# Optimization experiments

Measured on AMD Instinct MI355X. Metric: run time of the kernel, lower is better.

The kernel has to match this reference:

```python
import jax, jax.numpy as jnp
import numpy as np

HEADS = 8

def _grid_edges(H, W):
    # 4-neighbor grid adjacency, built at trace time (static), faithful to the torch double loop
    N = H * W
    idx = np.arange(N).reshape(H, W)
    e = np.zeros((N, N), np.float32)
    a, b = idx[1:, :].ravel(), idx[:-1, :].ravel()
    e[a, b] = 1.0; e[b, a] = 1.0
    a, b = idx[:, 1:].ravel(), idx[:, :-1].ravel()
    e[a, b] = 1.0; e[b, a] = 1.0
    return jnp.asarray(e)

def _layernorm(x, g, b, eps=1e-5):
    m = x.mean(-1, keepdims=True)
    v = x.var(-1, keepdims=True)
    return (x - m) / jnp.sqrt(v + eps) * g + b

def _gat(nodes, edges, W, b, rel):
    # nodes: [N,B,E]; W: [4,E,E] (q,k,v,out); rel: [HEADS]
    N, B, E = nodes.shape
    hd = E // HEADS
    q = (nodes @ W[0].T + b[0]).reshape(N, B, HEADS, hd)
    k = (nodes @ W[1].T + b[1]).reshape(N, B, HEADS, hd)
    v = (nodes @ W[2].T + b[2]).reshape(N, B, HEADS, hd)
    s = jnp.einsum('ibhd,jbhd->hbij', q, k) / float(np.sqrt(hd))
    s = s + edges[None, None] * rel[:, None, None, None]  # per-head edge relation bias
    a = jax.nn.softmax(s, axis=1)  # faithful to source: softmax over dim=1 (batch axis)
    o = jnp.einsum('hbij,jbhd->ibhd', a, v).reshape(N, B, E)
    return o @ W[3].T + b[3]

def _mha(q_in, kv_in, W, b):
    # standard nn.MultiheadAttention (eval, no dropout); seq-first [L,B,E]
    L, B, E = q_in.shape
    S = kv_in.shape[0]
    hd = E // HEADS
    q = (q_in @ W[0].T + b[0]).reshape(L, B, HEADS, hd)
    k = (kv_in @ W[1].T + b[1]).reshape(S, B, HEADS, hd)
    v = (kv_in @ W[2].T + b[2]).reshape(S, B, HEADS, hd)
    s = jnp.einsum('ibhd,jbhd->hbij', q, k) / float(np.sqrt(hd))
    a = jax.nn.softmax(s, axis=-1)
    o = jnp.einsum('hbij,jbhd->ibhd', a, v).reshape(L, B, E)
    return o @ W[3].T + b[3]

def reference(x, gat_W, gat_b, gat_rel, cross_W, cross_b, ln_g, ln_b):
    B, C, H, W = x.shape
    P = H // 4
    # global nodes: avg_pool2d(kernel=4) then flatten to [P*P, B, C]
    g = x.reshape(B, C, P, 4, P, 4).mean(axis=(3, 5))
    global_nodes = g.reshape(B, C, P * P).transpose(2, 0, 1)
    global_edges = jnp.ones((P * P, P * P), x.dtype)
    local_nodes = x.reshape(B, C, H * W).transpose(2, 0, 1)  # [HW,B,C]
    local_edges = _grid_edges(H, W)
    g_out = _gat(global_nodes, global_edges, gat_W[0], gat_b[0], gat_rel[0])
    g_out = _layernorm(g_out + global_nodes, ln_g[0], ln_b[0])
    l_out = _gat(local_nodes, local_edges, gat_W[1], gat_b[1], gat_rel[1])
    l_out = _layernorm(l_out + local_nodes, ln_g[1], ln_b[1])
    # nearest upsample x4 of global output back to HxW
    g_map = g_out.transpose(1, 2, 0).reshape(B, C, P, P)
    g_up = jnp.repeat(jnp.repeat(g_map, 4, axis=2), 4, axis=3)
    g_up = g_up.reshape(B, C, H * W).transpose(2, 0, 1)
    c_out = _mha(l_out, g_up, cross_W, cross_b)
    c_out = _layernorm(c_out + l_out, ln_g[2], ln_b[2])
    return c_out.transpose(1, 2, 0).reshape(B, C, H, W)

def setup_inputs() -> dict:
    key = jax.random.key(0)
    ks = jax.random.split(key, 6)
    B, C, H, W = 2, 256, 40, 40
    E = C
    sc = 0.02
    return {
        "x": jax.random.normal(ks[0], (B, C, H, W), jnp.float32),
        "gat_W": jax.random.normal(ks[1], (2, 4, E, E), jnp.float32) * sc,
        "gat_b": jax.random.normal(ks[2], (2, 4, E), jnp.float32) * sc,
        "gat_rel": jax.random.normal(ks[3], (2, HEADS), jnp.float32),
        "cross_W": jax.random.normal(ks[4], (4, E, E), jnp.float32) * sc,
        "cross_b": jax.random.normal(ks[5], (4, E), jnp.float32) * sc,
        "ln_g": jnp.ones((3, E), jnp.float32),
        "ln_b": jnp.zeros((3, E), jnp.float32),
    }
```

## Files before the change

### kernel.cpp

```cpp
#include <hip/hip_runtime.h>
#include <math.h>

#define NLOC 1600
#define NGLO 100

typedef unsigned short u16;
typedef short s16x8 __attribute__((ext_vector_type(8)));
typedef float f32x4 __attribute__((ext_vector_type(4)));

__device__ __forceinline__ short f2bf(float f) {
    unsigned u = __float_as_uint(f);
    u += 0x7fffu + ((u >> 16) & 1u);
    return (short)(u >> 16);
}
__device__ __forceinline__ float bf2f(u16 h) {
    return __uint_as_float(((unsigned)h) << 16);
}

__global__ __launch_bounds__(256) void wconv_kernel(const float* __restrict__ w1,
                                                    const float* __restrict__ w2,
                                                    u16* __restrict__ d1,
                                                    u16* __restrict__ d2) {
    int t = blockIdx.x * 256 + threadIdx.x;
    const float* src; u16* dst; int idx;
    if (t < 131072) { src = w1; dst = d1; idx = t; }
    else            { src = w2; dst = d2; idx = t - 131072; }
    float4 v = ((const float4*)src)[idx];
    ushort4 o;
    o.x = (u16)f2bf(v.x); o.y = (u16)f2bf(v.y);
    o.z = (u16)f2bf(v.z); o.w = (u16)f2bf(v.w);
    ((ushort4*)dst)[idx] = o;
}

__global__ __launch_bounds__(256) void prep_kernel(const float* __restrict__ x,
                                                   float* __restrict__ nodes,
                                                   u16* __restrict__ nodesb,
                                                   float* __restrict__ gn,
                                                   u16* __restrict__ gnb) {
    int bid = blockIdx.x;
    if (bid < 3200) {
        int t = bid * 256 + threadIdx.x;
        int c = t & 255;
        int b = (t >> 8) & 1;
        int n = t >> 9;
        float v = x[((size_t)(b * 256 + c)) * 1600 + n];
        nodes[t] = v;
        nodesb[t] = (u16)f2bf(v);
    } else {
        int t = (bid - 3200) * 256 + threadIdx.x;
        int c = t & 255;
        int b = (t >> 8) & 1;
        int n = t >> 9;
        int p = n / 10, qq = n - p * 10;
        const float* xp = x + ((size_t)(b * 256 + c)) * 1600 + (p * 4) * 40 + qq * 4;
        float s = 0.f;
#pragma unroll
        for (int dy = 0; dy < 4; ++dy)
#pragma unroll
            for (int dx = 0; dx < 4; ++dx)
                s += xp[dy * 40 + dx];
        s *= (1.f / 16.f);
        gn[t] = s;
        gnb[t] = (u16)f2bf(s);
    }
}

template <bool BF16OUT>
__global__ __launch_bounds__(64) void gemm_mfma(const u16* __restrict__ A,
                                                const u16* __restrict__ W,
                                                const float* __restrict__ bias,
                                                void* __restrict__ Cout, int M) {
    int z = blockIdx.z;
    W    += (size_t)z * 65536;
    bias += (size_t)z * 256;
    int lane = threadIdx.x;
    int c = lane & 15, qd = lane >> 4;
    int m0 = blockIdx.x * 32, n0 = blockIdx.y * 64;
    size_t co = (size_t)z * M * 256;

    f32x4 acc[2][4] = {};
#pragma unroll 2
    for (int kc = 0; kc < 8; ++kc) {
        int ko = kc * 32 + qd * 8;
        s16x8 af[2], bf[4];
#pragma unroll
        for (int mi = 0; mi < 2; ++mi) {
            int row = m0 + mi * 16 + c;
            s16x8 zz = {};
            af[mi] = (row < M) ? *(const s16x8*)(A + (size_t)row * 256 + ko) : zz;
        }
#pragma unroll
        for (int ni = 0; ni < 4; ++ni)
            bf[ni] = *(const s16x8*)(W + (size_t)(n0 + ni * 16 + c) * 256 + ko);
#pragma unroll
        for (int mi = 0; mi < 2; ++mi)
#pragma unroll
            for (int ni = 0; ni < 4; ++ni)
                acc[mi][ni] = __builtin_amdgcn_mfma_f32_16x16x32_bf16(af[mi], bf[ni],
                                                                      acc[mi][ni], 0, 0, 0);
    }
#pragma unroll
    for (int mi = 0; mi < 2; ++mi) {
#pragma unroll
        for (int r = 0; r < 4; ++r) {
            int row = m0 + mi * 16 + 4 * qd + r;
            if (row < M) {
#pragma unroll
                for (int ni = 0; ni < 4; ++ni) {
                    int col = n0 + ni * 16 + c;
                    float val = acc[mi][ni][r] + bias[col];
                    if (BF16OUT)
                        ((u16*)Cout)[co + (size_t)row * 256 + col] = (u16)f2bf(val);
                    else
                        ((float*)Cout)[co + (size_t)row * 256 + col] = val;
                }
            }
        }
    }
}

__global__ __launch_bounds__(256) void vtrans_kernel(const u16* __restrict__ src,
                                                     u16* __restrict__ dst,
                                                     int M, int Npad) {
    __shared__ u16 tile[32][33];
    int m0 = blockIdx.x * 32;
    int e0 = blockIdx.y * 32;
    int tx = threadIdx.x & 31, ty = threadIdx.x >> 5;
#pragma unroll
    for (int k2 = 0; k2 < 4; ++k2) {
        int m = m0 + ty + k2 * 8;
        tile[ty + k2 * 8][tx] = (m < M) ? src[(size_t)m * 256 + e0 + tx] : (u16)0;
    }
    __syncthreads();
    int b = tx >> 4, nl = tx & 15;
    int n = (m0 >> 1) + nl;
    if (n < Npad) {
#pragma unroll
        for (int k2 = 0; k2 < 4; ++k2) {
            int e = e0 + ty + k2 * 8;
            dst[(size_t)(b * 256 + e) * Npad + n] = tile[2 * nl + b][ty + k2 * 8];
        }
    }
}

__global__ __launch_bounds__(64) void colsum_kernel(const u16* __restrict__ vt,
                                                    float* __restrict__ sumv1,
                                                    int Npad) {
    int e = blockIdx.x;
    const u16* row = vt + (size_t)(256 + e) * Npad;
    float s = 0.f;
    for (int n = threadIdx.x; n < Npad; n += 64) s += bf2f(row[n]);
#pragma unroll
    for (int off = 1; off < 64; off <<= 1) s += __shfl_xor(s, off);
    if (threadIdx.x == 0) sumv1[e] = s;
}

struct KV { s16x8 kf[2][2]; s16x8 vf[2][2]; };

__global__ __launch_bounds__(64) void gat_attn_mfma(
    const u16* __restrict__ qb, const u16* __restrict__ kb,
    const u16* __restrict__ vt, const float* __restrict__ sumv1,
    u16* __restrict__ out, int N, int Npad, int nIT)
{
    __shared__ short At[16][40];
    int lane = threadIdx.x;
    int c  = lane & 15;
    int qd = lane >> 4;
    int h  = blockIdx.x / nIT;
    int it = blockIdx.x - h * nIT;
    int i0 = it * 16;
    int hb = h * 32;

    s16x8 qf0 = {}, qf1 = {};
    int i = i0 + c;
    if (i < N) {
        const u16* qp = qb + ((size_t)i * 2) * 256 + hb + qd * 8;
        qf0 = *(const s16x8*)qp;
        qf1 = *(const s16x8*)(qp + 256);
    }
#pragma unroll
    for (int z = 0; z < 8; ++z) qf0[z] ^= (short)0x8000;

    f32x4 o0[2] = {};
    f32x4 t1[2] = {};

    auto load_kv = [&](KV& B, int j0) {
#pragma unroll
        for (int b = 0; b < 2; ++b)
#pragma unroll
            for (int js = 0; js < 2; ++js) {
                int j = j0 + js * 16 + c;
                s16x8 kv = {};
                if (j < N) kv = *(const s16x8*)(kb + ((size_t)j * 2 + b) * 256 + hb + qd * 8);
                B.kf[b][js] = kv;
            }
#pragma unroll
        for (int b = 0; b < 2; ++b)
#pragma unroll
            for (int dh = 0; dh < 2; ++dh)
                B.vf[b][dh] = *(const s16x8*)(vt + (size_t)(b * 256 + hb + dh * 16 + c) * Npad
                                              + j0 + qd * 8);
    };

    auto compute = [&](KV& B) {
        f32x4 z4 = {};
        f32x4 sd0 = __builtin_amdgcn_mfma_f32_16x16x32_bf16(qf0, B.kf[0][0], z4, 0, 0, 0);
        sd0       = __builtin_amdgcn_mfma_f32_16x16x32_bf16(qf1, B.kf[1][0], sd0, 0, 0, 0);
        f32x4 sd1 = __builtin_amdgcn_mfma_f32_16x16x32_bf16(qf0, B.kf[0][1], z4, 0, 0, 0);
        sd1       = __builtin_amdgcn_mfma_f32_16x16x32_bf16(qf1, B.kf[1][1], sd1, 0, 0, 0);
#pragma unroll
        for (int r = 0; r < 4; ++r) {
            float e0v = __expf(sd0[r] * 0.17677669529663687f);
            At[4 * qd + r][c]      = f2bf(__builtin_amdgcn_rcpf(1.f + e0v));
            float e1v = __expf(sd1[r] * 0.17677669529663687f);
            At[4 * qd + r][16 + c] = f2bf(__builtin_amdgcn_rcpf(1.f + e1v));
        }
        asm volatile("s_waitcnt lgkmcnt(0)" ::: "memory");
        s16x8 af = *(const s16x8*)&At[c][qd * 8];
        o0[0] = __builtin_amdgcn_mfma_f32_16x16x32_bf16(af, B.vf[0][0], o0[0], 0, 0, 0);
        o0[1] = __builtin_amdgcn_mfma_f32_16x16x32_bf16(af, B.vf[0][1], o0[1], 0, 0, 0);
        t1[0] = __builtin_amdgcn_mfma_f32_16x16x32_bf16(af, B.vf[1][0], t1[0], 0, 0, 0);
        t1[1] = __builtin_amdgcn_mfma_f32_16x16x32_bf16(af, B.vf[1][1], t1[1], 0, 0, 0);
    };

    KV B0, B1;
    load_kv(B0, 0);
    for (int j0 = 0; j0 < N; j0 += 64) {
        bool h1 = (j0 + 32 < N);
        if (h1) load_kv(B1, j0 + 32);
        compute(B0);
        if (h1) {
            if (j0 + 64 < N) load_kv(B0, j0 + 64);
            compute(B1);
        }
    }

#pragma unroll
    for (int dh = 0; dh < 2; ++dh) {
        float sv = sumv1[hb + dh * 16 + c];
#pragma unroll
        for (int r = 0; r < 4; ++r) {
            int ii = i0 + 4 * qd + r;
            if (ii < N) {
                size_t o = ((size_t)ii * 2) * 256 + hb + dh * 16 + c;
                out[o]       = (u16)f2bf(o0[dh][r]);
                out[o + 256] = (u16)f2bf(sv - t1[dh][r]);
            }
        }
    }
}

__global__ __launch_bounds__(256) void lgat_attn(
    const u16* __restrict__ qb, const u16* __restrict__ kb,
    const u16* __restrict__ vt, float* __restrict__ pO, float* __restrict__ pT)
{
    __shared__ u16 ks[2][32][40];
    __shared__ u16 vs[2][32][40];
    __shared__ short At[4][16][40];

    int tid = threadIdx.x;
    int w = tid >> 6, lane = tid & 63;
    int c = lane & 15, qd = lane >> 4;
    int bx = blockIdx.x;
    int q4 = bx & 3;
    int hic = bx >> 2;
    int ic = hic % 25, h = hic / 25;
    int hb = h * 32;
    int i0 = ic * 64 + w * 16;
    int jb0 = q4 * 13, jbe = (jb0 + 13 < 50) ? jb0 + 13 : 50;

    const u16* qp = qb + ((size_t)(i0 + c) * 2) * 256 + hb + qd * 8;
    s16x8 qf0 = *(const s16x8*)qp;
    s16x8 qf1 = *(const s16x8*)(qp + 256);
#pragma unroll
    for (int z = 0; z < 8; ++z) qf0[z] ^= (short)0x8000;

    f32x4 o0[2] = {}, t1[2] = {};

    int srow = tid >> 2, part = tid & 3;
    int sjl = srow >> 1, sb = srow & 1;
    int vb_ = srow >> 5, vd = srow & 31;

    for (int jb = jb0; jb < jbe; ++jb) {
        int j0 = jb * 32;
        __syncthreads();
        {
            s16x8 kv = *(const s16x8*)(kb + (size_t)(j0 + sjl) * 512 + sb * 256 + hb + part * 8);
            *(s16x8*)&ks[sb][sjl][part * 8] = kv;
            s16x8 vv = *(const s16x8*)(vt + (size_t)(vb_ * 256 + hb + vd) * 1600 + j0 + part * 8);
            *(s16x8*)&vs[vb_][vd][part * 8] = vv;
        }
        __syncthreads();

        s16x8 kf00 = *(const s16x8*)&ks[0][c][qd * 8];
        s16x8 kf10 = *(const s16x8*)&ks[1][c][qd * 8];
        s16x8 kf01 = *(const s16x8*)&ks[0][16 + c][qd * 8];
        s16x8 kf11 = *(const s16x8*)&ks[1][16 + c][qd * 8];

        f32x4 z4 = {};
        f32x4 sd0 = __builtin_amdgcn_mfma_f32_16x16x32_bf16(qf0, kf00, z4, 0, 0, 0);
        sd0       = __builtin_amdgcn_mfma_f32_16x16x32_bf16(qf1, kf10, sd0, 0, 0, 0);
        f32x4 sd1 = __builtin_amdgcn_mfma_f32_16x16x32_bf16(qf0, kf01, z4, 0, 0, 0);
        sd1       = __builtin_amdgcn_mfma_f32_16x16x32_bf16(qf1, kf11, sd1, 0, 0, 0);
#pragma unroll
        for (int r = 0; r < 4; ++r) {
            float e0v = __expf(sd0[r] * 0.17677669529663687f);
            At[w][4 * qd + r][c]      = f2bf(__builtin_amdgcn_rcpf(1.f + e0v));
            float e1v = __expf(sd1[r] * 0.17677669529663687f);
            At[w][4 * qd + r][16 + c] = f2bf(__builtin_amdgcn_rcpf(1.f + e1v));
        }
        asm volatile("s_waitcnt lgkmcnt(0)" ::: "memory");
        s16x8 af = *(const s16x8*)&At[w][c][qd * 8];

        s16x8 vf00 = *(const s16x8*)&vs[0][c][qd * 8];
        s16x8 vf01 = *(const s16x8*)&vs[0][16 + c][qd * 8];
        s16x8 vf10 = *(const s16x8*)&vs[1][c][qd * 8];
        s16x8 vf11 = *(const s16x8*)&vs[1][16 + c][qd * 8];

        o0[0] = __builtin_amdgcn_mfma_f32_16x16x32_bf16(af, vf00, o0[0], 0, 0, 0);
        o0[1] = __builtin_amdgcn_mfma_f32_16x16x32_bf16(af, vf01, o0[1], 0, 0, 0);
        t1[0] = __builtin_amdgcn_mfma_f32_16x16x32_bf16(af, vf10, t1[0], 0, 0, 0);
        t1[1] = __builtin_amdgcn_mfma_f32_16x16x32_bf16(af, vf11, t1[1], 0, 0, 0);
    }

    size_t base = (size_t)q4 * 409600;
#pragma unroll
    for (int dh = 0; dh < 2; ++dh)
#pragma unroll
        for (int r = 0; r < 4; ++r) {
            size_t idx = base + (size_t)(i0 + 4 * qd + r) * 256 + hb + dh * 16 + c;
            pO[idx] = o0[dh][r];
            pT[idx] = t1[dh][r];
        }
}

__global__ __launch_bounds__(256) void lgat_combine(const float* __restrict__ pO,
                                                    const float* __restrict__ pT,
                                                    const float* __restrict__ sumv1,
                                                    u16* __restrict__ out) {
    int t = blockIdx.x * 256 + threadIdx.x;
    int e = t & 255;
    int i = t >> 8;
    float o  = pO[t] + pO[t + 409600] + pO[t + 819200] + pO[t + 1228800];
    float tt = pT[t] + pT[t + 409600] + pT[t + 819200] + pT[t + 1228800];
    out[(size_t)i * 512 + e]       = (u16)f2bf(o);
    out[(size_t)i * 512 + 256 + e] = (u16)f2bf(sumv1[e] - tt);
}

__global__ __launch_bounds__(64) void cross_attn_mfma(
    const u16* __restrict__ qb, const u16* __restrict__ kb,
    const u16* __restrict__ vt, u16* __restrict__ out)
{
    __shared__ short At[16][136];
    int lane = threadIdx.x;
    int c  = lane & 15;
    int qd = lane >> 4;
    int bx = blockIdx.x;
    int it = bx % 100;
    int hb2 = bx / 100;
    int h = hb2 >> 1, b = hb2 & 1;
    int i0 = it * 16;
    int hb = h * 32;

    for (int z = lane; z < 16 * 24; z += 64)
        At[z / 24][112 + (z % 24)] = 0;

    const u16* qp = qb + ((size_t)(i0 + c) * 2 + b) * 256 + hb + qd * 8;
    s16x8 qf = *(const s16x8*)qp;

    f32x4 s[7];
#pragma unroll
    for (int jt = 0; jt < 7; ++jt) {
        int j = jt * 16 + c;
        s16x8 kf = {};
        if (j < NGLO) kf = *(const s16x8*)(kb + ((size_t)j * 2 + b) * 256 + hb + qd * 8);
        f32x4 z4 = {};
        s[jt] = __builtin_amdgcn_mfma_f32_16x16x32_bf16(qf, kf, z4, 0, 0, 0);
    }
    if (c >= 4) {
#pragma unroll
// ... 19 lines not shown
        for (int jt = 0; jt < 7; ++jt) {
            float p = __expf(s[jt][r] - mm);
            s[jt][r] = p;
            ll += p;
        }
        ll += __shfl_xor(ll, 1);
        ll += __shfl_xor(ll, 2);
        ll += __shfl_xor(ll, 4);
        ll += __shfl_xor(ll, 8);
        l[r] = ll;
    }
#pragma unroll
    for (int jt = 0; jt < 7; ++jt)
#pragma unroll
        for (int r = 0; r < 4; ++r)
            At[4 * qd + r][jt * 16 + c] = f2bf(s[jt][r]);
    asm volatile("s_waitcnt lgkmcnt(0)" ::: "memory");

    f32x4 o[2] = {};
#pragma unroll
    for (int kc = 0; kc < 4; ++kc) {
        s16x8 af = *(const s16x8*)&At[c][kc * 32 + qd * 8];
#pragma unroll
        for (int dh = 0; dh < 2; ++dh) {
            s16x8 vf = *(const s16x8*)(vt + (size_t)(b * 256 + hb + dh * 16 + c) * 128
                                       + kc * 32 + qd * 8);
            o[dh] = __builtin_amdgcn_mfma_f32_16x16x32_bf16(af, vf, o[dh], 0, 0, 0);
        }
    }
#pragma unroll
    for (int dh = 0; dh < 2; ++dh)
#pragma unroll
        for (int r = 0; r < 4; ++r) {
            int ii = i0 + 4 * qd + r;
            out[((size_t)ii * 2 + b) * 256 + hb + dh * 16 + c] = (u16)f2bf(o[dh][r] / l[r]);
        }
}

__global__ __launch_bounds__(256) void ln_kernel(const float* __restrict__ P,
                                                 const float* __restrict__ R,
                                                 const float* __restrict__ g,
                                                 const float* __restrict__ bb,
                                                 float* __restrict__ out,
                                                 u16* __restrict__ outb, int mode) {
    int r = blockIdx.x;
    int c = threadIdx.x;
    size_t o = (size_t)r * 256 + c;
    float x = P[o] + R[o];
    float s1 = x, s2 = x * x;
#pragma unroll
    for (int off = 1; off < 64; off <<= 1) {
        s1 += __shfl_xor(s1, off);
        s2 += __shfl_xor(s2, off);
    }
    __shared__ float w1[4], w2[4];
    int wid = c >> 6;
    if ((c & 63) == 0) { w1[wid] = s1; w2[wid] = s2; }
    __syncthreads();
    s1 = w1[0] + w1[1] + w1[2] + w1[3];
    s2 = w2[0] + w2[1] + w2[2] + w2[3];
    float mean = s1 * (1.f / 256.f);
    float var  = s2 * (1.f / 256.f) - mean * mean;
    float y = (x - mean) * rsqrtf(var + 1e-5f) * g[c] + bb[c];
    if (mode == 0) {
        out[o] = y;
        if (outb) outb[o] = (u16)f2bf(y);
    } else {
        int n = r >> 1, b = r & 1;
        out[((size_t)(b * 256 + c)) * 1600 + n] = y;
    }
}

extern "C" void kernel_launch(void* const* d_in, const int* in_sizes, int n_in,
                              void* d_out, int out_size, void* d_ws, size_t ws_size,
                              hipStream_t stream) {
    const float* x        = (const float*)d_in[0];
    const float* gat_W    = (const float*)d_in[1];
    const float* gat_b    = (const float*)d_in[2];
    const float* cross_W  = (const float*)d_in[4];
    const float* cross_b  = (const float*)d_in[5];
    const float* ln_g     = (const float*)d_in[6];
    const float* ln_b     = (const float*)d_in[7];
    float* out = (float*)d_out;

    float* ws    = (float*)d_ws;
// ... 22 lines not shown
    u16* gvt    = gvb + 51200;
    u16* gattb  = gvt + 65536;
    u16* goutb  = gattb + 51200;
    u16* ckb    = goutb + 51200;
    u16* cvb    = ckb + 51200;
    u16* cvt    = cvb + 51200;
    u16* loutb  = vbuf;
    u16* cqb    = attb;
    u16* cattb  = kbuf;

    const u16* W0b = wgatb;
    const u16* W1b = wgatb + 4 * 65536;
    const float* b0 = gat_b;
    const float* b1 = gat_b + 4 * 256;

    wconv_kernel<<<768, 256, 0, stream>>>(gat_W, cross_W, wgatb, wcrsb);
    prep_kernel<<<3400, 256, 0, stream>>>(x, nodes, nodesb, gn, gnb);

    gemm_mfma<true><<<dim3(7, 4, 3), 64, 0, stream>>>(gnb, W0b, b0, gqb, 200);
    vtrans_kernel<<<dim3(8, 8), 256, 0, stream>>>(gvb, gvt, 200, 128);
    colsum_kernel<<<256, 64, 0, stream>>>(gvt, sv1g, 128);
    gat_attn_mfma<<<8 * 7, 64, 0, stream>>>(gqb, gkb, gvt, sv1g, gattb, NGLO, 128, 7);
    gemm_mfma<false><<<dim3(7, 4, 1), 64, 0, stream>>>(gattb, W0b + 3 * 65536, b0 + 768, gprj, 200);
    ln_kernel<<<200, 256, 0, stream>>>(gprj, gn, ln_g, ln_b, gout, goutb, 0);

    gemm_mfma<true><<<dim3(100, 4, 3), 64, 0, stream>>>(nodesb, W1b, b1, qbuf, 3200);
    vtrans_kernel<<<dim3(100, 8), 256, 0, stream>>>(vbuf, vtb, 3200, 1600);
    colsum_kernel<<<256, 64, 0, stream>>>(vtb, sv1l, 1600);
    lgat_attn<<<800, 256, 0, stream>>>(qbuf, kbuf, vtb, pO, pT);
    lgat_combine<<<1600, 256, 0, stream>>>(pO, pT, sv1l, attb);
    gemm_mfma<false><<<dim3(100, 4, 1), 64, 0, stream>>>(attb, W1b + 3 * 65536, b1 + 768, proj, 3200);
    ln_kernel<<<3200, 256, 0, stream>>>(proj, nodes, ln_g + 256, ln_b + 256, lout, loutb, 0);

    gemm_mfma<true><<<dim3(100, 4, 1), 64, 0, stream>>>(loutb, wcrsb, cross_b, cqb, 3200);
    gemm_mfma<true><<<dim3(7, 4, 2), 64, 0, stream>>>(goutb, wcrsb + 1 * 65536, cross_b + 256, ckb, 200);
    vtrans_kernel<<<dim3(8, 8), 256, 0, stream>>>(cvb, cvt, 200, 128);
    cross_attn_mfma<<<1600, 64, 0, stream>>>(cqb, ckb, cvt, cattb);
    gemm_mfma<false><<<dim3(100, 4, 1), 64, 0, stream>>>(cattb, wcrsb + 3 * 65536, cross_b + 768, proj, 3200);
    ln_kernel<<<3200, 256, 0, stream>>>(proj, lout, ln_g + 512, ln_b + 512, out, (u16*)0, 1);
}
```

Baseline: 201.5 us.

## Fuse pipeline into fewer kernels with GEMM+LayerNorm epilogues and merged branches

Collapses about twenty launches into nine by merging the global and local branches into shared grids. The column sums move into the V-transpose via atomics, and the output projections are fused with residual add and LayerNorm in a full-row per-wave GEMM epilogue. The cross attention now packs four waves per block. This cuts launch overhead and the fp32 intermediate round trips through memory. In exchange, the projection+LN kernels run on very few blocks (for example 50 or 64), which may underuse the GPU.

```diff
diff --git a/kernel.cpp b/kernel.cpp
--- a/kernel.cpp
+++ b/kernel.cpp
@@ -17,27 +17,135 @@
     return __uint_as_float(((unsigned)h) << 16);
 }
 
-__global__ __launch_bounds__(256) void wconv_kernel(const float* __restrict__ w1,
-                                                    const float* __restrict__ w2,
-                                                    u16* __restrict__ d1,
-                                                    u16* __restrict__ d2) {
-    int t = blockIdx.x * 256 + threadIdx.x;
-    const float* src; u16* dst; int idx;
-    if (t < 131072) { src = w1; dst = d1; idx = t; }
-    else            { src = w2; dst = d2; idx = t - 131072; }
-    float4 v = ((const float4*)src)[idx];
-    ushort4 o;
-    o.x = (u16)f2bf(v.x); o.y = (u16)f2bf(v.y);
-    o.z = (u16)f2bf(v.z); o.w = (u16)f2bf(v.w);
-    ((ushort4*)dst)[idx] = o;
-}
-
-__global__ __launch_bounds__(256) void prep_kernel(const float* __restrict__ x,
-                                                   float* __restrict__ nodes,
-                                                   u16* __restrict__ nodesb,
-                                                   float* __restrict__ gn,
-                                                   u16* __restrict__ gnb) {
-    int bid = blockIdx.x;
+
+__device__ __forceinline__ void gemm_tile(int lane, const u16* __restrict__ A,
+                                          const u16* __restrict__ W,
+                                          const float* __restrict__ bias,
+                                          u16* __restrict__ C, int M, int m0, int n0) {
+    int c = lane & 15, qd = lane >> 4;
+    f32x4 acc[2][4] = {};
+#pragma unroll 2
+    for (int kc = 0; kc < 8; ++kc) {
+        int ko = kc * 32 + qd * 8;
+        s16x8 af[2], bf[4];
+#pragma unroll
+        for (int mi = 0; mi < 2; ++mi) {
+            int row = m0 + mi * 16 + c;
+            s16x8 zz = {};
+            af[mi] = (row < M) ? *(const s16x8*)(A + (size_t)row * 256 + ko) : zz;
+        }
+#pragma unroll
+        for (int ni = 0; ni < 4; ++ni)
+            bf[ni] = *(const s16x8*)(W + (size_t)(n0 + ni * 16 + c) * 256 + ko);
+#pragma unroll
+        for (int mi = 0; mi < 2; ++mi)
+#pragma unroll
+            for (int ni = 0; ni < 4; ++ni)
+                acc[mi][ni] = __builtin_amdgcn_mfma_f32_16x16x32_bf16(af[mi], bf[ni],
+                                                                      acc[mi][ni], 0, 0, 0);
+    }
+#pragma unroll
+    for (int mi = 0; mi < 2; ++mi)
+#pragma unroll
+        for (int r = 0; r < 4; ++r) {
+            int row = m0 + mi * 16 + 4 * qd + r;
+            if (row < M) {
+#pragma unroll
+                for (int ni = 0; ni < 4; ++ni) {
+                    int col = n0 + ni * 16 + c;
+                    C[(size_t)row * 256 + col] = (u16)f2bf(acc[mi][ni][r] + bias[col]);
+                }
+            }
+        }
+}
+
+__device__ __forceinline__ void gemmln_wave(int lane, const u16* __restrict__ A,
+                                            const u16* __restrict__ W,
+                                            const float* __restrict__ bias,
+                                            const float* __restrict__ R,
+                                            const float* __restrict__ g,
+                                            const float* __restrict__ bb,
+                                            float* fout, u16* bfout, float* dout,
+                                            int M, int m0, int mode) {
+    int c = lane & 15, qd = lane >> 4;
+    f32x4 acc[16] = {};
+#pragma unroll 2
+    for (int kc = 0; kc < 8; ++kc) {
+        int ko = kc * 32 + qd * 8;
+        int row = m0 + c;
+        s16x8 zz = {};
+        s16x8 af = (row < M) ? *(const s16x8*)(A + (size_t)row * 256 + ko) : zz;
+#pragma unroll
+        for (int ni = 0; ni < 16; ++ni) {
+            s16x8 bf = *(const s16x8*)(W + (size_t)(ni * 16 + c) * 256 + ko);
+            acc[ni] = __builtin_amdgcn_mfma_f32_16x16x32_bf16(af, bf, acc[ni], 0, 0, 0);
+        }
+    }
+#pragma unroll
+    for (int r = 0; r < 4; ++r) {
+        int row = m0 + 4 * qd + r;
+        bool ok = (row < M);
+        float v[16];
+        float s1 = 0.f, s2 = 0.f;
+#pragma unroll
+        for (int ni = 0; ni < 16; ++ni) {
+            int col = ni * 16 + c;
+            float val = acc[ni][r] + bias[col] + (ok ? R[(size_t)row * 256 + col] : 0.f);
+            v[ni] = val;
+            s1 += val; s2 += val * val;
+        }
+        s1 += __shfl_xor(s1, 1); s2 += __shfl_xor(s2, 1);
+        s1 += __shfl_xor(s1, 2); s2 += __shfl_xor(s2, 2);
+        s1 += __shfl_xor(s1, 4); s2 += __shfl_xor(s2, 4);
+        s1 += __shfl_xor(s1, 8); s2 += __shfl_xor(s2, 8);
+        float mean = s1 * (1.f / 256.f);
+        float var  = s2 * (1.f / 256.f) - mean * mean;
+        float rstd = rsqrtf(var + 1e-5f);
+        if (ok) {
+            if (mode == 0) {
+#pragma unroll
+                for (int ni = 0; ni < 16; ++ni) {
+                    int col = ni * 16 + c;
+                    float y = (v[ni] - mean) * rstd * g[col] + bb[col];
+                    fout[(size_t)row * 256 + col] = y;
+                    bfout[(size_t)row * 256 + col] = (u16)f2bf(y);
+                }
+            } else {
+                int n = row >> 1, b = row & 1;
+#pragma unroll
+                for (int ni = 0; ni < 16; ++ni) {
+                    int col = ni * 16 + c;
+                    float y = (v[ni] - mean) * rstd * g[col] + bb[col];
+                    dout[((size_t)(b * 256 + col)) * 1600 + n] = y;
+                }
+            }
+        }
+    }
+}
+
+__global__ __launch_bounds__(256) void k_prep(const float* __restrict__ gw,
+                                              const float* __restrict__ cw,
+                                              u16* __restrict__ gwb,
+                                              u16* __restrict__ cwb,
+                                              const float* __restrict__ x,
+                                              float* __restrict__ nodes,
+                                              u16* __restrict__ nodesb,
+                                              float* __restrict__ gn,
+                                              u16* __restrict__ gnb) {
+    int bx = blockIdx.x;
+    if (bx < 768) {
+        int t = bx * 256 + threadIdx.x;
+        const float* src; u16* dst; int idx;
+        if (t < 131072) { src = gw; dst = gwb; idx = t; }
+        else            { src = cw; dst = cwb; idx = t - 131072; }
+        float4 v = ((const float4*)src)[idx];
+        ushort4 o;
+        o.x = (u16)f2bf(v.x); o.y = (u16)f2bf(v.y);
+        o.z = (u16)f2bf(v.z); o.w = (u16)f2bf(v.w);
+        ((ushort4*)dst)[idx] = o;
+        return;
+    }
+    int bid = bx - 768;
     if (bid < 3200) {
         int t = bid * 256 + threadIdx.x;
         int c = t & 255;
@@ -65,66 +173,37 @@
     }
 }
 
-template <bool BF16OUT>
-__global__ __launch_bounds__(64) void gemm_mfma(const u16* __restrict__ A,
-                                                const u16* __restrict__ W,
-                                                const float* __restrict__ bias,
-                                                void* __restrict__ Cout, int M) {
-    int z = blockIdx.z;
-    W    += (size_t)z * 65536;
-    bias += (size_t)z * 256;
+__global__ __launch_bounds__(64) void k_qkv(const u16* __restrict__ nodesb,
+                                            const u16* __restrict__ gnb,
+                                            const u16* __restrict__ W1b,
+                                            const u16* __restrict__ W0b,
+                                            const float* __restrict__ b1,
+                                            const float* __restrict__ b0,
+                                            u16* __restrict__ qbuf,
+                                            u16* __restrict__ gqb,
+                                            float* __restrict__ sv1) {
     int lane = threadIdx.x;
-    int c = lane & 15, qd = lane >> 4;
-    int m0 = blockIdx.x * 32, n0 = blockIdx.y * 64;
-    size_t co = (size_t)z * M * 256;
-
-    f32x4 acc[2][4] = {};
-#pragma unroll 2
-    for (int kc = 0; kc < 8; ++kc) {
-        int ko = kc * 32 + qd * 8;
-        s16x8 af[2], bf[4];
-#pragma unroll
-        for (int mi = 0; mi < 2; ++mi) {
-            int row = m0 + mi * 16 + c;
-            s16x8 zz = {};
-            af[mi] = (row < M) ? *(const s16x8*)(A + (size_t)row * 256 + ko) : zz;
-        }
-#pragma unroll
-        for (int ni = 0; ni < 4; ++ni)
-            bf[ni] = *(const s16x8*)(W + (size_t)(n0 + ni * 16 + c) * 256 + ko);
-#pragma unroll
-        for (int mi = 0; mi < 2; ++mi)
-#pragma unroll
-            for (int ni = 0; ni < 4; ++ni)
-                acc[mi][ni] = __builtin_amdgcn_mfma_f32_16x16x32_bf16(af[mi], bf[ni],
-                                                                      acc[mi][ni], 0, 0, 0);
-    }
-#pragma unroll
-    for (int mi = 0; mi < 2; ++mi) {
-#pragma unroll
-        for (int r = 0; r < 4; ++r) {
-            int row = m0 + mi * 16 + 4 * qd + r;
-            if (row < M) {
-#pragma unroll
-                for (int ni = 0; ni < 4; ++ni) {
-                    int col = n0 + ni * 16 + c;
-                    float val = acc[mi][ni][r] + bias[col];
-                    if (BF16OUT)
-                        ((u16*)Cout)[co + (size_t)row * 256 + col] = (u16)f2bf(val);
-                    else
-                        ((float*)Cout)[co + (size_t)row * 256 + col] = val;
-                }
-            }
-        }
-    }
-}
-
-__global__ __launch_bounds__(256) void vtrans_kernel(const u16* __restrict__ src,
-                                                     u16* __restrict__ dst,
-                                                     int M, int Npad) {
+    int bx = blockIdx.x, z = blockIdx.z;
+    int n0 = blockIdx.y * 64;
+    if (bx == 100 && blockIdx.y == 0 && z == 0) {
+#pragma unroll
+        for (int i = 0; i < 8; ++i) sv1[lane * 8 + i] = 0.f;
+    }
+    if (bx < 100)
+        gemm_tile(lane, nodesb, W1b + (size_t)z * 65536, b1 + z * 256,
+                  qbuf + (size_t)z * 819200, 3200, bx * 32, n0);
+    else
+        gemm_tile(lane, gnb, W0b + (size_t)z * 65536, b0 + z * 256,
+                  gqb + (size_t)z * 51200, 200, (bx - 100) * 32, n0);
+}
+
+__device__ __forceinline__ void vtrans_block(const u16* __restrict__ src,
+                                             u16* __restrict__ dst,
+                                             int M, int Npad, int bxx, int byy,
+                                             float* sum) {
     __shared__ u16 tile[32][33];
-    int m0 = blockIdx.x * 32;
-    int e0 = blockIdx.y * 32;
+    int m0 = bxx * 32;
+    int e0 = byy * 32;
     int tx = threadIdx.x & 31, ty = threadIdx.x >> 5;
 #pragma unroll
     for (int k2 = 0; k2 < 4; ++k2) {
@@ -141,229 +220,296 @@
             dst[(size_t)(b * 256 + e) * Npad + n] = tile[2 * nl + b][ty + k2 * 8];
         }
     }
-}
-
-__global__ __launch_bounds__(64) void colsum_kernel(const u16* __restrict__ vt,
-                                                    float* __restrict__ sumv1,
-                                                    int Npad) {
-    int e = blockIdx.x;
-    const u16* row = vt + (size_t)(256 + e) * Npad;
-    float s = 0.f;
-    for (int n = threadIdx.x; n < Npad; n += 64) s += bf2f(row[n]);
-#pragma unroll
-    for (int off = 1; off < 64; off <<= 1) s += __shfl_xor(s, off);
-    if (threadIdx.x == 0) sumv1[e] = s;
-}
-
-struct KV { s16x8 kf[2][2]; s16x8 vf[2][2]; };
-
-__global__ __launch_bounds__(64) void gat_attn_mfma(
+    if (threadIdx.x < 32) {
+        float s = 0.f;
+#pragma unroll
+        for (int r = 0; r < 16; ++r) s += bf2f(tile[2 * r + 1][threadIdx.x]);
+        atomicAdd(&sum[e0 + threadIdx.x], s);
+    }
+}
+
+__global__ __launch_bounds__(256) void k_vtrans(const u16* __restrict__ vbuf,
+                                                u16* __restrict__ vtb,
+                                                const u16* __restrict__ gvb,
+                                                u16* __restrict__ gvt,
+                                                float* __restrict__ sv1l,
+                                                float* __restrict__ sv1g) {
+    int bx = blockIdx.x;
+    if (bx < 100) vtrans_block(vbuf, vtb, 3200, 1600, bx, blockIdx.y, sv1l);
+    else          vtrans_block(gvb, gvt, 200, 128, bx - 100, blockIdx.y, sv1g);
+}
+
+__global__ __launch_bounds__(256) void k_attn(
     const u16* __restrict__ qb, const u16* __restrict__ kb,
-    const u16* __restrict__ vt, const float* __restrict__ sumv1,
-    u16* __restrict__ out, int N, int Npad, int nIT)
-{
-    __shared__ short At[16][40];
-    int lane = threadIdx.x;
-    int c  = lane & 15;
-    int qd = lane >> 4;
-    int h  = blockIdx.x / nIT;
-    int it = blockIdx.x - h * nIT;
-    int i0 = it * 16;
-    int hb = h * 32;
-
-    s16x8 qf0 = {}, qf1 = {};
-    int i = i0 + c;
-    if (i < N) {
-        const u16* qp = qb + ((size_t)i * 2) * 256 + hb + qd * 8;
-        qf0 = *(const s16x8*)qp;
-        qf1 = *(const s16x8*)(qp + 256);
-    }
-#pragma unroll
-    for (int z = 0; z < 8; ++z) qf0[z] ^= (short)0x8000;
-
-    f32x4 o0[2] = {};
-    f32x4 t1[2] = {};
-
-    auto load_kv = [&](KV& B, int j0) {
-#pragma unroll
-        for (int b = 0; b < 2; ++b)
-#pragma unroll
-            for (int js = 0; js < 2; ++js) {
-                int j = j0 + js * 16 + c;
-                s16x8 kv = {};
-                if (j < N) kv = *(const s16x8*)(kb + ((size_t)j * 2 + b) * 256 + hb + qd * 8);
-                B.kf[b][js] = kv;
-            }
-#pragma unroll
-        for (int b = 0; b < 2; ++b)
-#pragma unroll
-            for (int dh = 0; dh < 2; ++dh)
-                B.vf[b][dh] = *(const s16x8*)(vt + (size_t)(b * 256 + hb + dh * 16 + c) * Npad
-                                              + j0 + qd * 8);
-    };
-
-    auto compute = [&](KV& B) {
-        f32x4 z4 = {};
-        f32x4 sd0 = __builtin_amdgcn_mfma_f32_16x16x32_bf16(qf0, B.kf[0][0], z4, 0, 0, 0);
-        sd0       = __builtin_amdgcn_mfma_f32_16x16x32_bf16(qf1, B.kf[1][0], sd0, 0, 0, 0);
-        f32x4 sd1 = __builtin_amdgcn_mfma_f32_16x16x32_bf16(qf0, B.kf[0][1], z4, 0, 0, 0);
-        sd1       = __builtin_amdgcn_mfma_f32_16x16x32_bf16(qf1, B.kf[1][1], sd1, 0, 0, 0);
-#pragma unroll
-        for (int r = 0; r < 4; ++r) {
-            float e0v = __expf(sd0[r] * 0.17677669529663687f);
-            At[4 * qd + r][c]      = f2bf(__builtin_amdgcn_rcpf(1.f + e0v));
-            float e1v = __expf(sd1[r] * 0.17677669529663687f);
-            At[4 * qd + r][16 + c] = f2bf(__builtin_amdgcn_rcpf(1.f + e1v));
-        }
-        asm volatile("s_waitcnt lgkmcnt(0)" ::: "memory");
-        s16x8 af = *(const s16x8*)&At[c][qd * 8];
-        o0[0] = __builtin_amdgcn_mfma_f32_16x16x32_bf16(af, B.vf[0][0], o0[0], 0, 0, 0);
-        o0[1] = __builtin_amdgcn_mfma_f32_16x16x32_bf16(af, B.vf[0][1], o0[1], 0, 0, 0);
-        t1[0] = __builtin_amdgcn_mfma_f32_16x16x32_bf16(af, B.vf[1][0], t1[0], 0, 0, 0);
-        t1[1] = __builtin_amdgcn_mfma_f32_16x16x32_bf16(af, B.vf[1][1], t1[1], 0, 0, 0);
-    };
-
-    KV B0, B1;
-    load_kv(B0, 0);
-    for (int j0 = 0; j0 < N; j0 += 64) {
-        bool h1 = (j0 + 32 < N);
-        if (h1) load_kv(B1, j0 + 32);
-        compute(B0);
-        if (h1) {
-            if (j0 + 64 < N) load_kv(B0, j0 + 64);
-            compute(B1);
-        }
-    }
-
-#pragma unroll
-    for (int dh = 0; dh < 2; ++dh) {
-        float sv = sumv1[hb + dh * 16 + c];
-#pragma unroll
-        for (int r = 0; r < 4; ++r) {
-            int ii = i0 + 4 * qd + r;
-            if (ii < N) {
-                size_t o = ((size_t)ii * 2) * 256 + hb + dh * 16 + c;
-                out[o]       = (u16)f2bf(o0[dh][r]);
-                out[o + 256] = (u16)f2bf(sv - t1[dh][r]);
-            }
-        }
-    }
-}
-
-__global__ __launch_bounds__(256) void lgat_attn(
-    const u16* __restrict__ qb, const u16* __restrict__ kb,
-    const u16* __restrict__ vt, float* __restrict__ pO, float* __restrict__ pT)
+    const u16* __restrict__ vt, float* __restrict__ pO, float* __restrict__ pT,
+    const u16* __restrict__ gqb, const u16* __restrict__ gkb,
+    const u16* __restrict__ gvt, const float* __restrict__ sv1g,
+    u16* __restrict__ gattb)
 {
     __shared__ u16 ks[2][32][40];
     __shared__ u16 vs[2][32][40];
-    __shared__ short At[4][16][40];
+    __shared__ short At4[4][16][40];
 
     int tid = threadIdx.x;
     int w = tid >> 6, lane = tid & 63;
     int c = lane & 15, qd = lane >> 4;
     int bx = blockIdx.x;
-    int q4 = bx & 3;
-    int hic = bx >> 2;
-    int ic = hic % 25, h = hic / 25;
-    int hb = h * 32;
-    int i0 = ic * 64 + w * 16;
-    int jb0 = q4 * 13, jbe = (jb0 + 13 < 50) ? jb0 + 13 : 50;
-
-    const u16* qp = qb + ((size_t)(i0 + c) * 2) * 256 + hb + qd * 8;
-    s16x8 qf0 = *(const s16x8*)qp;
-    s16x8 qf1 = *(const s16x8*)(qp + 256);
-#pragma unroll
-    for (int z = 0; z < 8; ++z) qf0[z] ^= (short)0x8000;
-
-    f32x4 o0[2] = {}, t1[2] = {};
-
-    int srow = tid >> 2, part = tid & 3;
-    int sjl = srow >> 1, sb = srow & 1;
-    int vb_ = srow >> 5, vd = srow & 31;
-
-    for (int jb = jb0; jb < jbe; ++jb) {
-        int j0 = jb * 32;
+
+    if (bx < 800) {
+        int q4 = bx & 3;
+        int hic = bx >> 2;
+        int ic = hic % 25, h = hic / 25;
+        int hb = h * 32;
+        int i0 = ic * 64 + w * 16;
+        int jb0 = q4 * 13, jbe = (jb0 + 13 < 50) ? jb0 + 13 : 50;
+
+        const u16* qp = qb + ((size_t)(i0 + c) * 2) * 256 + hb + qd * 8;
+        s16x8 qf0 = *(const s16x8*)qp;
+        s16x8 qf1 = *(const s16x8*)(qp + 256);
+#pragma unroll
+        for (int z = 0; z < 8; ++z) qf0[z] ^= (short)0x8000;
+
+        f32x4 o0[2] = {}, t1[2] = {};
+
+        int srow = tid >> 2, part = tid & 3;
+        int sjl = srow >> 1, sb = srow & 1;
+        int vb_ = srow >> 5, vd = srow & 31;
+
+        for (int jb = jb0; jb < jbe; ++jb) {
+            int j0 = jb * 32;
+            __syncthreads();
+            {
+                s16x8 kv = *(const s16x8*)(kb + (size_t)(j0 + sjl) * 512 + sb * 256 + hb + part * 8);
+                *(s16x8*)&ks[sb][sjl][part * 8] = kv;
+                s16x8 vv = *(const s16x8*)(vt + (size_t)(vb_ * 256 + hb + vd) * 1600 + j0 + part * 8);
+                *(s16x8*)&vs[vb_][vd][part * 8] = vv;
+            }
+            __syncthreads();
+
+            s16x8 kf00 = *(const s16x8*)&ks[0][c][qd * 8];
+            s16x8 kf10 = *(const s16x8*)&ks[1][c][qd * 8];
+            s16x8 kf01 = *(const s16x8*)&ks[0][16 + c][qd * 8];
+            s16x8 kf11 = *(const s16x8*)&ks[1][16 + c][qd * 8];
+
+            f32x4 z4 = {};
+            f32x4 sd0 = __builtin_amdgcn_mfma_f32_16x16x32_bf16(qf0, kf00, z4, 0, 0, 0);
+            sd0       = __builtin_amdgcn_mfma_f32_16x16x32_bf16(qf1, kf10, sd0, 0, 0, 0);
+            f32x4 sd1 = __builtin_amdgcn_mfma_f32_16x16x32_bf16(qf0, kf01, z4, 0, 0, 0);
+            sd1       = __builtin_amdgcn_mfma_f32_16x16x32_bf16(qf1, kf11, sd1, 0, 0, 0);
+#pragma unroll
+            for (int r = 0; r < 4; ++r) {
+                float e0v = __expf(sd0[r] * 0.17677669529663687f);
+                At4[w][4 * qd + r][c]      = f2bf(__builtin_amdgcn_rcpf(1.f + e0v));
+                float e1v = __expf(sd1[r] * 0.17677669529663687f);
+                At4[w][4 * qd + r][16 + c] = f2bf(__builtin_amdgcn_rcpf(1.f + e1v));
+            }
+            asm volatile("s_waitcnt lgkmcnt(0)" ::: "memory");
+            s16x8 af = *(const s16x8*)&At4[w][c][qd * 8];
+
+            s16x8 vf00 = *(const s16x8*)&vs[0][c][qd * 8];
+            s16x8 vf01 = *(const s16x8*)&vs[0][16 + c][qd * 8];
+            s16x8 vf10 = *(const s16x8*)&vs[1][c][qd * 8];
+            s16x8 vf11 = *(const s16x8*)&vs[1][16 + c][qd * 8];
+
+            o0[0] = __builtin_amdgcn_mfma_f32_16x16x32_bf16(af, vf00, o0[0], 0, 0, 0);
+            o0[1] = __builtin_amdgcn_mfma_f32_16x16x32_bf16(af, vf01, o0[1], 0, 0, 0);
+            t1[0] = __builtin_amdgcn_mfma_f32_16x16x32_bf16(af, vf10, t1[0], 0, 0, 0);
+            t1[1] = __builtin_amdgcn_mfma_f32_16x16x32_bf16(af, vf11, t1[1], 0, 0, 0);
+        }
+
+        size_t base = (size_t)q4 * 409600;
+#pragma unroll
+        for (int dh = 0; dh < 2; ++dh)
+#pragma unroll
+            for (int r = 0; r < 4; ++r) {
+                size_t idx = base + (size_t)(i0 + 4 * qd + r) * 256 + hb + dh * 16 + c;
+                pO[idx] = o0[dh][r];
+                pT[idx] = t1[dh][r];
+            }
+    } else {
+        int idx = (bx - 800) * 4 + w;
+        int h = idx / 7, it = idx % 7;
+        int i0 = it * 16;
+        int hb = h * 32;
+
+        s16x8 qf0 = {}, qf1 = {};
+        int i = i0 + c;
+        if (i < NGLO) {
+            const u16* qp = gqb + ((size_t)i * 2) * 256 + hb + qd * 8;
+            qf0 = *(const s16x8*)qp;
+            qf1 = *(const s16x8*)(qp + 256);
+        }
+#pragma unroll
+        for (int z = 0; z < 8; ++z) qf0[z] ^= (short)0x8000;
+
+        f32x4 o0[2] = {}, t1[2] = {};
+
+        for (int j0 = 0; j0 < NGLO; j0 += 32) {
+            s16x8 kf[2][2], vf[2][2];
+#pragma unroll
+            for (int b = 0; b < 2; ++b)
+#pragma unroll
+                for (int js = 0; js < 2; ++js) {
+                    int j = j0 + js * 16 + c;
+                    s16x8 kv = {};
+                    if (j < NGLO) kv = *(const s16x8*)(gkb + ((size_t)j * 2 + b) * 256 + hb + qd * 8);
+                    kf[b][js] = kv;
+                }
+#pragma unroll
+            for (int b = 0; b < 2; ++b)
+#pragma unroll
+                for (int dh = 0; dh < 2; ++dh)
+                    vf[b][dh] = *(const s16x8*)(gvt + (size_t)(b * 256 + hb + dh * 16 + c) * 128
+                                                + j0 + qd * 8);
+
+            f32x4 z4 = {};
+            f32x4 sd0 = __builtin_amdgcn_mfma_f32_16x16x32_bf16(qf0, kf[0][0], z4, 0, 0, 0);
+            sd0       = __builtin_amdgcn_mfma_f32_16x16x32_bf16(qf1, kf[1][0], sd0, 0, 0, 0);
+            f32x4 sd1 = __builtin_amdgcn_mfma_f32_16x16x32_bf16(qf0, kf[0][1], z4, 0, 0, 0);
+            sd1       = __builtin_amdgcn_mfma_f32_16x16x32_bf16(qf1, kf[1][1], sd1, 0, 0, 0);
+#pragma unroll
+            for (int r = 0; r < 4; ++r) {
+                float e0v = __expf(sd0[r] * 0.17677669529663687f);
+                At4[w][4 * qd + r][c]      = f2bf(__builtin_amdgcn_rcpf(1.f + e0v));
+                float e1v = __expf(sd1[r] * 0.17677669529663687f);
+                At4[w][4 * qd + r][16 + c] = f2bf(__builtin_amdgcn_rcpf(1.f + e1v));
+            }
+            asm volatile("s_waitcnt lgkmcnt(0)" ::: "memory");
+            s16x8 af = *(const s16x8*)&At4[w][c][qd * 8];
+            o0[0] = __builtin_amdgcn_mfma_f32_16x16x32_bf16(af, vf[0][0], o0[0], 0, 0, 0);
+            o0[1] = __builtin_amdgcn_mfma_f32_16x16x32_bf16(af, vf[0][1], o0[1], 0, 0, 0);
+            t1[0] = __builtin_amdgcn_mfma_f32_16x16x32_bf16(af, vf[1][0], t1[0], 0, 0, 0);
+            t1[1] = __builtin_amdgcn_mfma_f32_16x16x32_bf16(af, vf[1][1], t1[1], 0, 0, 0);
+        }
+
+#pragma unroll
+        for (int dh = 0; dh < 2; ++dh) {
+            float sv = sv1g[hb + dh * 16 + c];
+#pragma unroll
+            for (int r = 0; r < 4; ++r) {
+                int ii = i0 + 4 * qd + r;
+                if (ii < NGLO) {
+                    size_t o = ((size_t)ii * 2) * 256 + hb + dh * 16 + c;
+                    gattb[o]       = (u16)f2bf(o0[dh][r]);
+                    gattb[o + 256] = (u16)f2bf(sv - t1[dh][r]);
+                }
+            }
+        }
+    }
+}
+
+__global__ __launch_bounds__(256) void k_combine_gproj(
+    const float* __restrict__ pO, const float* __restrict__ pT,
+    const float* __restrict__ sv1l, u16* __restrict__ attb,
+    const u16* __restrict__ gattb, const u16* __restrict__ W0p,
+    const float* __restrict__ b0p, const float* __restrict__ gn,
+    const float* __restrict__ ln_g, const float* __restrict__ ln_b,
+    float* __restrict__ gout, u16* __restrict__ goutb)
+{
+    int bx = blockIdx.x;
+    if (bx < 400) {
+        int t4 = (bx * 256 + threadIdx.x) * 4;
+        int e = t4 & 255;
+        int i = t4 >> 8;
+        float4 o  = *(const float4*)(pO + t4);
+        float4 tt = *(const float4*)(pT + t4);
+#pragma unroll
+        for (int q = 1; q < 4; ++q) {
+            float4 a = *(const float4*)(pO + t4 + q * 409600);
+            float4 b = *(const float4*)(pT + t4 + q * 409600);
+            o.x += a.x; o.y += a.y; o.z += a.z; o.w += a.w;
+            tt.x += b.x; tt.y += b.y; tt.z += b.z; tt.w += b.w;
+        }
+        float4 sv = *(const float4*)(sv1l + e);
+        ushort4 w0, w1;
+        w0.x = (u16)f2bf(o.x); w0.y = (u16)f2bf(o.y);
+        w0.z = (u16)f2bf(o.z); w0.w = (u16)f2bf(o.w);
+        w1.x = (u16)f2bf(sv.x - tt.x); w1.y = (u16)f2bf(sv.y - tt.y);
+        w1.z = (u16)f2bf(sv.z - tt.z); w1.w = (u16)f2bf(sv.w - tt.w);
+        *(ushort4*)(attb + (size_t)i * 512 + e)       = w0;
+        *(ushort4*)(attb + (size_t)i * 512 + 256 + e) = w1;
+    } else {
+        int w = threadIdx.x >> 6, lane = threadIdx.x & 63;
+        int idx = (bx - 400) * 4 + w;
+        if (idx < 13)
+            gemmln_wave(lane, gattb, W0p, b0p, gn, ln_g, ln_b,
+                        gout, goutb, (float*)0, 200, idx * 16, 0);
+    }
+}
+
+__global__ __launch_bounds__(256) void k_lproj_ckcv(
+    const u16* __restrict__ attb, const u16* __restrict__ W1p,
+    const float* __restrict__ b1p, const float* __restrict__ nodes,
+    const float* __restrict__ ln_g1, const float* __restrict__ ln_b1,
+    float* __restrict__ lout, u16* __restrict__ loutb,
+    const u16* __restrict__ goutb, const u16* __restrict__ wckv,
+    const float* __restrict__ bckv, u16* __restrict__ ckb)
+{
+    int bx = blockIdx.x;
+    int w = threadIdx.x >> 6, lane = threadIdx.x & 63;
+    if (bx < 50) {
+        int idx = bx * 4 + w;
+        gemmln_wave(lane, attb, W1p, b1p, nodes, ln_g1, ln_b1,
+                    lout, loutb, (float*)0, 3200, idx * 16, 0);
+    } else {
+        int idx = (bx - 50) * 4 + w;
+        int z = idx / 28, rem = idx % 28;
+        int m0 = (rem >> 2) * 32, n0 = (rem & 3) * 64;
+        gemm_tile(lane, goutb, wckv + (size_t)z * 65536, bckv + z * 256,
+                  ckb + (size_t)z * 51200, 200, m0, n0);
+    }
+}
+
+__global__ __launch_bounds__(256) void k_cq_vtrans(
+    const u16* __restrict__ loutb, const u16* __restrict__ wcq,
+    const float* __restrict__ bcq, u16* __restrict__ cqb,
+    const u16* __restrict__ cvb, u16* __restrict__ cvt)
+{
+    int bx = blockIdx.x;
+    if (bx < 100) {
+        int w = threadIdx.x >> 6, lane = threadIdx.x & 63;
+        int idx = bx * 4 + w;
+        int m0 = (idx % 100) * 32, n0 = (idx / 100) * 64;
+        gemm_tile(lane, loutb, wcq, bcq, cqb, 3200, m0, n0);
+    } else {
+        int bb = bx - 100;
+        __shared__ u16 tile[32][33];
+        int m0 = (bb & 7) * 32;
+        int e0 = (bb >> 3) * 32;
+        int tx = threadIdx.x & 31, ty = threadIdx.x >> 5;
+#pragma unroll
+        for (int k2 = 0; k2 < 4; ++k2) {
+            int m = m0 + ty + k2 * 8;
+            tile[ty + k2 * 8][tx] = (m < 200) ? cvb[(size_t)m * 256 + e0 + tx] : (u16)0;
+        }
         __syncthreads();
-        {
-            s16x8 kv = *(const s16x8*)(kb + (size_t)(j0 + sjl) * 512 + sb * 256 + hb + part * 8);
-            *(s16x8*)&ks[sb][sjl][part * 8] = kv;
-            s16x8 vv = *(const s16x8*)(vt + (size_t)(vb_ * 256 + hb + vd) * 1600 + j0 + part * 8);
-            *(s16x8*)&vs[vb_][vd][part * 8] = vv;
-        }
-        __syncthreads();
-
-        s16x8 kf00 = *(const s16x8*)&ks[0][c][qd * 8];
-        s16x8 kf10 = *(const s16x8*)&ks[1][c][qd * 8];
-        s16x8 kf01 = *(const s16x8*)&ks[0][16 + c][qd * 8];
-        s16x8 kf11 = *(const s16x8*)&ks[1][16 + c][qd * 8];
-
-        f32x4 z4 = {};
-        f32x4 sd0 = __builtin_amdgcn_mfma_f32_16x16x32_bf16(qf0, kf00, z4, 0, 0, 0);
-        sd0       = __builtin_amdgcn_mfma_f32_16x16x32_bf16(qf1, kf10, sd0, 0, 0, 0);
-        f32x4 sd1 = __builtin_amdgcn_mfma_f32_16x16x32_bf16(qf0, kf01, z4, 0, 0, 0);
-        sd1       = __builtin_amdgcn_mfma_f32_16x16x32_bf16(qf1, kf11, sd1, 0, 0, 0);
-#pragma unroll
-        for (int r = 0; r < 4; ++r) {
-            float e0v = __expf(sd0[r] * 0.17677669529663687f);
-            At[w][4 * qd + r][c]      = f2bf(__builtin_amdgcn_rcpf(1.f + e0v));
-            float e1v = __expf(sd1[r] * 0.17677669529663687f);
-            At[w][4 * qd + r][16 + c] = f2bf(__builtin_amdgcn_rcpf(1.f + e1v));
-        }
-        asm volatile("s_waitcnt lgkmcnt(0)" ::: "memory");
-        s16x8 af = *(const s16x8*)&At[w][c][qd * 8];
-
-        s16x8 vf00 = *(const s16x8*)&vs[0][c][qd * 8];
-        s16x8 vf01 = *(const s16x8*)&vs[0][16 + c][qd * 8];
-        s16x8 vf10 = *(const s16x8*)&vs[1][c][qd * 8];
-        s16x8 vf11 = *(const s16x8*)&vs[1][16 + c][qd * 8];
-
-        o0[0] = __builtin_amdgcn_mfma_f32_16x16x32_bf16(af, vf00, o0[0], 0, 0, 0);
-        o0[1] = __builtin_amdgcn_mfma_f32_16x16x32_bf16(af, vf01, o0[1], 0, 0, 0);
-        t1[0] = __builtin_amdgcn_mfma_f32_16x16x32_bf16(af, vf10, t1[0], 0, 0, 0);
-        t1[1] = __builtin_amdgcn_mfma_f32_16x16x32_bf16(af, vf11, t1[1], 0, 0, 0);
-    }
-
-    size_t base = (size_t)q4 * 409600;
-#pragma unroll
-    for (int dh = 0; dh < 2; ++dh)
-#pragma unroll
-        for (int r = 0; r < 4; ++r) {
-            size_t idx = base + (size_t)(i0 + 4 * qd + r) * 256 + hb + dh * 16 + c;
-            pO[idx] = o0[dh][r];
-            pT[idx] = t1[dh][r];
-        }
-}
-
-__global__ __launch_bounds__(256) void lgat_combine(const float* __restrict__ pO,
-                                                    const float* __restrict__ pT,
-                                                    const float* __restrict__ sumv1,
-                                                    u16* __restrict__ out) {
-    int t = blockIdx.x * 256 + threadIdx.x;
-    int e = t & 255;
-    int i = t >> 8;
-    float o  = pO[t] + pO[t + 409600] + pO[t + 819200] + pO[t + 1228800];
-    float tt = pT[t] + pT[t + 409600] + pT[t + 819200] + pT[t + 1228800];
-    out[(size_t)i * 512 + e]       = (u16)f2bf(o);
-    out[(size_t)i * 512 + 256 + e] = (u16)f2bf(sumv1[e] - tt);
-}
-
-__global__ __launch_bounds__(64) void cross_attn_mfma(
+        int b = tx >> 4, nl = tx & 15;
+        int n = (m0 >> 1) + nl;
+#pragma unroll
+        for (int k2 = 0; k2 < 4; ++k2) {
+            int e = e0 + ty + k2 * 8;
+            cvt[(size_t)(b * 256 + e) * 128 + n] = tile[2 * nl + b][ty + k2 * 8];
+        }
+    }
+}
+
+__global__ __launch_bounds__(256) void k_cross(
     const u16* __restrict__ qb, const u16* __restrict__ kb,
     const u16* __restrict__ vt, u16* __restrict__ out)
 {
-    __shared__ short At[16][136];
-    int lane = threadIdx.x;
+    __shared__ short At[4][16][136];
+    int w = threadIdx.x >> 6, lane = threadIdx.x & 63;
     int c  = lane & 15;
     int qd = lane >> 4;
-    int bx = blockIdx.x;
-    int it = bx % 100;
-    int hb2 = bx / 100;
+    int idx = blockIdx.x * 4 + w;
+    int it = idx % 100;
+    int hb2 = idx / 100;
     int h = hb2 >> 1, b = hb2 & 1;
     int i0 = it * 16;
     int hb = h * 32;
 
     for (int z = lane; z < 16 * 24; z += 64)
-        At[z / 24][112 + (z % 24)] = 0;
+        At[w][z / 24][112 + (z % 24)] = 0;
 
     const u16* qp = qb + ((size_t)(i0 + c) * 2 + b) * 256 + hb + qd * 8;
     s16x8 qf = *(const s16x8*)qp;
@@ -413,13 +559,13 @@
     for (int jt = 0; jt < 7; ++jt)
 #pragma unroll
         for (int r = 0; r < 4; ++r)
-            At[4 * qd + r][jt * 16 + c] = f2bf(s[jt][r]);
+            At[w][4 * qd + r][jt * 16 + c] = f2bf(s[jt][r]);
     asm volatile("s_waitcnt lgkmcnt(0)" ::: "memory");
 
     f32x4 o[2] = {};
 #pragma unroll
     for (int kc = 0; kc < 4; ++kc) {
-        s16x8 af = *(const s16x8*)&At[c][kc * 32 + qd * 8];
+        s16x8 af = *(const s16x8*)&At[w][c][kc * 32 + qd * 8];
 #pragma unroll
         for (int dh = 0; dh < 2; ++dh) {
             s16x8 vf = *(const s16x8*)(vt + (size_t)(b * 256 + hb + dh * 16 + c) * 128
@@ -436,38 +582,16 @@
         }
 }
 
-__global__ __launch_bounds__(256) void ln_kernel(const float* __restrict__ P,
-                                                 const float* __restrict__ R,
-                                                 const float* __restrict__ g,
-                                                 const float* __restrict__ bb,
-                                                 float* __restrict__ out,
-                                                 u16* __restrict__ outb, int mode) {
-    int r = blockIdx.x;
-    int c = threadIdx.x;
-    size_t o = (size_t)r * 256 + c;
-    float x = P[o] + R[o];
-    float s1 = x, s2 = x * x;
-#pragma unroll
-    for (int off = 1; off < 64; off <<= 1) {
-        s1 += __shfl_xor(s1, off);
-        s2 += __shfl_xor(s2, off);
-    }
-    __shared__ float w1[4], w2[4];
-    int wid = c >> 6;
-    if ((c & 63) == 0) { w1[wid] = s1; w2[wid] = s2; }
-    __syncthreads();
-    s1 = w1[0] + w1[1] + w1[2] + w1[3];
-    s2 = w2[0] + w2[1] + w2[2] + w2[3];
-    float mean = s1 * (1.f / 256.f);
-    float var  = s2 * (1.f / 256.f) - mean * mean;
-    float y = (x - mean) * rsqrtf(var + 1e-5f) * g[c] + bb[c];
-    if (mode == 0) {
-        out[o] = y;
-        if (outb) outb[o] = (u16)f2bf(y);
-    } else {
-        int n = r >> 1, b = r & 1;
-        out[((size_t)(b * 256 + c)) * 1600 + n] = y;
-    }
+__global__ __launch_bounds__(256) void k_cproj(
+    const u16* __restrict__ cattb, const u16* __restrict__ wcp,
+    const float* __restrict__ bcp, const float* __restrict__ lout,
+    const float* __restrict__ ln_g2, const float* __restrict__ ln_b2,
+    float* __restrict__ dout)
+{
+    int w = threadIdx.x >> 6, lane = threadIdx.x & 63;
+    int idx = blockIdx.x * 4 + w;
+    gemmln_wave(lane, cattb, wcp, bcp, lout, ln_g2, ln_b2,
+                (float*)0, (u16*)0, dout, 3200, idx * 16, 1);
 }
 
 extern "C" void kernel_launch(void* const* d_in, const int* in_sizes, int n_in,
@@ -520,28 +644,21 @@
     const float* b0 = gat_b;
     const float* b1 = gat_b + 4 * 256;
 
-    wconv_kernel<<<768, 256, 0, stream>>>(gat_W, cross_W, wgatb, wcrsb);
-    prep_kernel<<<3400, 256, 0, stream>>>(x, nodes, nodesb, gn, gnb);
-
-    gemm_mfma<true><<<dim3(7, 4, 3), 64, 0, stream>>>(gnb, W0b, b0, gqb, 200);
-    vtrans_kernel<<<dim3(8, 8), 256, 0, stream>>>(gvb, gvt, 200, 128);
-    colsum_kernel<<<256, 64, 0, stream>>>(gvt, sv1g, 128);
-    gat_attn_mfma<<<8 * 7, 64, 0, stream>>>(gqb, gkb, gvt, sv1g, gattb, NGLO, 128, 7);
-    gemm_mfma<false><<<dim3(7, 4, 1), 64, 0, stream>>>(gattb, W0b + 3 * 65536, b0 + 768, gprj, 200);
-    ln_kernel<<<200, 256, 0, stream>>>(gprj, gn, ln_g, ln_b, gout, goutb, 0);
-
-    gemm_mfma<true><<<dim3(100, 4, 3), 64, 0, stream>>>(nodesb, W1b, b1, qbuf, 3200);
-    vtrans_kernel<<<dim3(100, 8), 256, 0, stream>>>(vbuf, vtb, 3200, 1600);
-    colsum_kernel<<<256, 64, 0, stream>>>(vtb, sv1l, 1600);
-    lgat_attn<<<800, 256, 0, stream>>>(qbuf, kbuf, vtb, pO, pT);
-    lgat_combine<<<1600, 256, 0, stream>>>(pO, pT, sv1l, attb);
-    gemm_mfma<false><<<dim3(100, 4, 1), 64, 0, stream>>>(attb, W1b + 3 * 65536, b1 + 768, proj, 3200);
-    ln_kernel<<<3200, 256, 0, stream>>>(proj, nodes, ln_g + 256, ln_b + 256, lout, loutb, 0);
-
-    gemm_mfma<true><<<dim3(100, 4, 1), 64, 0, stream>>>(loutb, wcrsb, cross_b, cqb, 3200);
-    gemm_mfma<true><<<dim3(7, 4, 2), 64, 0, stream>>>(goutb, wcrsb + 1 * 65536, cross_b + 256, ckb, 200);
-    vtrans_kernel<<<dim3(8, 8), 256, 0, stream>>>(cvb, cvt, 200, 128);
-    cross_attn_mfma<<<1600, 64, 0, stream>>>(cqb, ckb, cvt, cattb);
-    gemm_mfma<false><<<dim3(100, 4, 1), 64, 0, stream>>>(cattb, wcrsb + 3 * 65536, cross_b + 768, proj, 3200);
-    ln_kernel<<<3200, 256, 0, stream>>>(proj, lout, ln_g + 512, ln_b + 512, out, (u16*)0, 1);
-}
+    k_prep<<<4168, 256, 0, stream>>>(gat_W, cross_W, wgatb, wcrsb,
+                                     x, nodes, nodesb, gn, gnb);
+    k_qkv<<<dim3(107, 4, 3), 64, 0, stream>>>(nodesb, gnb, W1b, W0b, b1, b0,
+                                              qbuf, gqb, sv1l);
+    k_vtrans<<<dim3(108, 8), 256, 0, stream>>>(vbuf, vtb, gvb, gvt, sv1l, sv1g);
+    k_attn<<<814, 256, 0, stream>>>(qbuf, kbuf, vtb, pO, pT,
+                                    gqb, gkb, gvt, sv1g, gattb);
+    k_combine_gproj<<<404, 256, 0, stream>>>(pO, pT, sv1l, attb,
+                                             gattb, W0b + 3 * 65536, b0 + 768, gn,
+                                             ln_g, ln_b, gout, goutb);
+    k_lproj_ckcv<<<64, 256, 0, stream>>>(attb, W1b + 3 * 65536, b1 + 768, nodes,
+                                         ln_g + 256, ln_b + 256, lout, loutb,
+                                         goutb, wcrsb + 65536, cross_b + 256, ckb);
+    k_cq_vtrans<<<164, 256, 0, stream>>>(loutb, wcrsb, cross_b, cqb, cvb, cvt);
+    k_cross<<<400, 256, 0, stream>>>(cqb, ckb, cvt, cattb);
+    k_cproj<<<50, 256, 0, stream>>>(cattb, wcrsb + 3 * 65536, cross_b + 768, lout,
+                                    ln_g + 512, ln_b + 512, out);
+}
```

Result: slower. 244.9 us (+21.6%).
